# Performance work log

Hardware: AMD Instinct MI355X
Metric: run time of the kernel (lower is better)

## Reference

```python
import jax, jax.numpy as jnp
import numpy as np

TEMPERATURE = 1.0
D_THRESH = 0.1
EPS = 1e-10
NORM_EPS = 1e-12  # F.normalize clamp


def _l2_normalize(x):
    n = jnp.sqrt(jnp.sum(x * x, axis=1, keepdims=True))
    return x / jnp.maximum(n, NORM_EPS)


def setup_inputs() -> dict:
    key = jax.random.key(0)
    k1, k2, k3 = jax.random.split(key, 3)
    N, D = 8192, 128
    f1 = jax.random.normal(k1, (N, D), dtype=jnp.float32)
    f2 = jax.random.normal(k2, (N, D), dtype=jnp.float32)
    # continuous targets in [-1, 1) so both the distance mask (|ti-tj|>0.1)
    # and the polarity mask (sign mismatch) are exercised
    targets = jax.random.uniform(k3, (N,), dtype=jnp.float32, minval=-1.0, maxval=1.0)
    return {"f1": f1, "f2": f2, "targets": targets}


def reference(f1, f2, targets):
    f1 = _l2_normalize(f1)
    f2 = _l2_normalize(f2)

    # self_mask: 1 where pair is a negative (far target or opposite polarity)
    dist_t = jnp.abs(targets[:, None] - targets[None, :])  # [N,N]
    mask_distance = dist_t > D_THRESH
    polarity = targets > 0
    mask_polarity = polarity[:, None] != polarity[None, :]
    self_mask = (mask_distance | mask_polarity).astype(f1.dtype)  # [N,N]

    # ||f1_i - f2_j||^2 via the cdist/matmul trick (avoids [N,N,D] tensor)
    sq1 = jnp.sum(f1 * f1, axis=1)  # [N]
    sq2 = jnp.sum(f2 * f2, axis=1)  # [N]
    dist = sq1[:, None] - 2.0 * (f1 @ f2.T) + sq2[None, :]  # [N,N]
    cos = 1.0 - 0.5 * dist

    p = jax.nn.softmax(cos / TEMPERATURE, axis=1)  # [N,N]
    pos_w = 1.0 - self_mask
    log_pos = -jnp.log(p + EPS) * pos_w
    log_neg = -jnp.log(1.0 - p + EPS) * self_mask
    per_row = (jnp.sum(log_pos, axis=1) / jnp.sum(pos_w, axis=1)
               + jnp.sum(log_neg, axis=1) / jnp.sum(self_mask, axis=1))
    return jnp.mean(per_row)
```

## Files before the change

### kernel.cpp

```cpp
#include <hip/hip_runtime.h>
#include <hip/hip_bf16.h>
#include <math.h>

#define NROWS 8192
#define DDIM  128
#define JCHUNKS 16
#define JPER  (NROWS / JCHUNKS)
#define STAGE_COLS 64
#define NSTAGES (JPER / STAGE_COLS)
#define ROWS_PER_BLOCK 128
#define GRIDX (NROWS / ROWS_PER_BLOCK)
#define LOG2E 1.44269504088896f

#define AS1 __attribute__((address_space(1)))
#define AS3 __attribute__((address_space(3)))

typedef __attribute__((ext_vector_type(8))) short bf16x8;
typedef __attribute__((ext_vector_type(4))) float f32x4;

__global__ __launch_bounds__(256) void norm_kernel(
    const float* __restrict__ f1, const float* __restrict__ f2,
    __hip_bfloat16* __restrict__ f1b, __hip_bfloat16* __restrict__ f2b,
    float* __restrict__ out) {
  if (blockIdx.x == 0 && threadIdx.x == 0) out[0] = 0.0f;
  int t = threadIdx.x;
  int rloc = t >> 5;
  int l = t & 31;
  int b = blockIdx.x;
  int half = (b >= NROWS / 8) ? 1 : 0;
  int row = (b - half * (NROWS / 8)) * 8 + rloc;
  const float* src = half ? f2 : f1;
  __hip_bfloat16* dst = half ? f2b : f1b;

  float4 v = ((const float4*)src)[row * (DDIM / 4) + l];
  float s = v.x * v.x + v.y * v.y + v.z * v.z + v.w * v.w;
  #pragma unroll
  for (int off = 1; off < 32; off <<= 1) s += __shfl_xor(s, off, 64);
  float inv = 1.0f / fmaxf(sqrtf(s), 1e-12f);
  __hip_bfloat16 hv[4];
  hv[0] = __float2bfloat16(v.x * inv);
  hv[1] = __float2bfloat16(v.y * inv);
  hv[2] = __float2bfloat16(v.z * inv);
  hv[3] = __float2bfloat16(v.w * inv);
  *(ushort4*)&dst[(size_t)row * DDIM + l * 4] = *(ushort4*)hv;
}

__global__ __launch_bounds__(128, 2) void stats_kernel(
    const __hip_bfloat16* __restrict__ f1b,
    const __hip_bfloat16* __restrict__ f2b,
    const float* __restrict__ targets,
    float* __restrict__ partials) {
  __shared__ __align__(16) char lds0[STAGE_COLS * 256];
  __shared__ __align__(16) char lds1[STAGE_COLS * 256];
  __shared__ __align__(16) float tsh[JPER];

  const int chunk = blockIdx.y;
  const int i0 = blockIdx.x * ROWS_PER_BLOCK;
  const int w    = threadIdx.x >> 6;
  const int lane = threadIdx.x & 63;
  const int p15  = lane & 15;
  const int rl4  = lane >> 4;
  const int rbase = i0 + w * 64;

  bf16x8 afrag[4][4];
  #pragma unroll
  for (int rs = 0; rs < 4; ++rs) {
    const __hip_bfloat16* arow =
        &f1b[(size_t)(rbase + rs * 16 + p15) * DDIM + rl4 * 8];
    #pragma unroll
    for (int ks = 0; ks < 4; ++ks)
      afrag[rs][ks] = *(const bf16x8*)(arow + ks * 32);
  }

  f32x4 ki[4];
  #pragma unroll
  for (int rs = 0; rs < 4; ++rs)
    #pragma unroll
    for (int rr = 0; rr < 4; ++rr)
      ki[rs][rr] = targets[rbase + rs * 16 + rl4 * 4 + rr];

  f32x4 Z[4], Zp[4], Cp[4], Np[4];
  #pragma unroll
  for (int rs = 0; rs < 4; ++rs) {
    Z[rs] = (f32x4){0.f, 0.f, 0.f, 0.f};
    Zp[rs] = (f32x4){0.f, 0.f, 0.f, 0.f};
    Cp[rs] = (f32x4){0.f, 0.f, 0.f, 0.f};
    Np[rs] = (f32x4){0.f, 0.f, 0.f, 0.f};
  }

  const int jb0 = chunk * JPER;

  int srcoff[8];
  #pragma unroll
  for (int q = 0; q < 8; ++q) {
    int rloc = w * 32 + q * 4 + rl4;
    int c    = p15 ^ ((q * 4 + rl4) & 15);
    srcoff[q] = rloc * DDIM + c * 8;
  }

  {
    #pragma unroll
    for (int rnd = 0; rnd < 4; ++rnd)
      __builtin_amdgcn_global_load_lds(
          (const AS1 void*)(targets + jb0 + rnd * 128 + threadIdx.x),
          (AS3 void*)(&tsh[rnd * 128 + w * 64]), 4, 0, 0);
    const __hip_bfloat16* gstage = f2b + (size_t)jb0 * DDIM;
    char* lbase = &lds0[w * 8192];
    #pragma unroll
    for (int q = 0; q < 8; ++q)
      __builtin_amdgcn_global_load_lds((const AS1 void*)(gstage + srcoff[q]),
                                       (AS3 void*)(lbase + q * 1024), 16, 0, 0);
  }

  for (int s = 0; s < NSTAGES; ++s) {
    __syncthreads();

    if (s + 1 < NSTAGES) {
      const __hip_bfloat16* gstage = f2b + (size_t)(jb0 + (s + 1) * STAGE_COLS) * DDIM;
      char* lbase = ((s + 1) & 1) ? &lds1[w * 8192] : &lds0[w * 8192];
      #pragma unroll
      for (int q = 0; q < 8; ++q)
        __builtin_amdgcn_global_load_lds((const AS1 void*)(gstage + srcoff[q]),
                                         (AS3 void*)(lbase + q * 1024), 16, 0, 0);
    }

    const char* lb = (s & 1) ? lds1 : lds0;
    #pragma unroll
    for (int ct = 0; ct < 4; ++ct) {
      const int rloc = ct * 16 + p15;
      bf16x8 bfrag[4];
      #pragma unroll
      for (int ks = 0; ks < 4; ++ks)
        bfrag[ks] = *(const bf16x8*)(lb + rloc * 256 + (((rl4 + ks * 4) ^ p15) << 4));

      float tj = tsh[s * STAGE_COLS + ct * 16 + p15];
      const bool pj = tj > 0.0f;
      const f32x4 tj4 = {tj, tj, tj, tj};
      const f32x4 K4  = {LOG2E, LOG2E, LOG2E, LOG2E};

      #pragma unroll
      for (int rs = 0; rs < 4; ++rs) {
        f32x4 acc = {0.f, 0.f, 0.f, 0.f};
        #pragma unroll
        for (int ks = 0; ks < 4; ++ks)
          acc = __builtin_amdgcn_mfma_f32_16x16x32_bf16(afrag[rs][ks], bfrag[ks], acc, 0, 0, 0);

        f32x4 c4 = acc;
        f32x4 d4 = ki[rs] - tj4;
        f32x4 m4;
        #pragma unroll
        for (int rr = 0; rr < 4; ++rr) {
          bool q = (__builtin_fabsf(d4[rr]) <= 0.1f) & ((ki[rs][rr] > 0.0f) == pj);
          m4[rr] = q ? 1.0f : 0.0f;
        }
        f32x4 x4 = c4 * K4 - K4;
        f32x4 e4;
        #pragma unroll
        for (int rr = 0; rr < 4; ++rr) e4[rr] = __builtin_amdgcn_exp2f(x4[rr]);
        Z[rs]  += e4;
        Zp[rs] += m4 * e4;
        Cp[rs] += m4 * c4;
        Np[rs] += m4;
      }
    }
  }

  #pragma unroll
  for (int rs = 0; rs < 4; ++rs) {
    #pragma unroll
    for (int rr = 0; rr < 4; ++rr) {
      #pragma unroll
      for (int off = 1; off < 16; off <<= 1) {
        Z[rs][rr]  += __shfl_xor(Z[rs][rr],  off, 64);
        Zp[rs][rr] += __shfl_xor(Zp[rs][rr], off, 64);
        Cp[rs][rr] += __shfl_xor(Cp[rs][rr], off, 64);
        Np[rs][rr] += __shfl_xor(Np[rs][rr], off, 64);
      }
    }
  }
  if (p15 == 0) {
    #pragma unroll
    for (int rs = 0; rs < 4; ++rs)
      #pragma unroll
      for (int rr = 0; rr < 4; ++rr) {
        size_t row = rbase + rs * 16 + rl4 * 4 + rr;
        f32x4 st = {Z[rs][rr], Zp[rs][rr], Cp[rs][rr], Np[rs][rr]};
        *(f32x4*)&partials[((size_t)row * JCHUNKS + chunk) * 4] = st;
      }
  }
}

__global__ void finalize_rows(const float* __restrict__ partials,
                              float* __restrict__ out) {
  int r = blockIdx.x * 256 + threadIdx.x;
  float Z = 0, Zp = 0, Cp = 0, Np = 0;
  for (int ch = 0; ch < JCHUNKS; ++ch) {
    float4 p = *(const float4*)&partials[((size_t)r * JCHUNKS + ch) * 4];
    Z += p.x; Zp += p.y; Cp += p.z; Np += p.w;
  }
  float Zn = Z - Zp;
  float nn = (float)NROWS - Np;
  float spos = (1.0f + logf(Z)) - Cp / Np;
  float sneg = Zn / Z - nn * 1e-10f;
  float per_row = spos + sneg / nn;

  float v = per_row;
  for (int off = 32; off; off >>= 1) v += __shfl_xor(v, off, 64);
  __shared__ float wsum[4];
  int lane = threadIdx.x & 63, wid = threadIdx.x >> 6;
  if (lane == 0) wsum[wid] = v;
  __syncthreads();
  if (threadIdx.x == 0)
    atomicAdd(out, (wsum[0] + wsum[1] + wsum[2] + wsum[3]) * (1.0f / (float)NROWS));
}

extern "C" void kernel_launch(void* const* d_in, const int* in_sizes, int n_in,
                              void* d_out, int out_size, void* d_ws, size_t ws_size,
                              hipStream_t stream) {
  const float* f1  = (const float*)d_in[0];
  const float* f2  = (const float*)d_in[1];
  const float* tgt = (const float*)d_in[2];
  float* out = (float*)d_out;

  char* ws = (char*)d_ws;
  __hip_bfloat16* f1b = (__hip_bfloat16*)ws;
  __hip_bfloat16* f2b = (__hip_bfloat16*)(ws + (size_t)NROWS * DDIM * 2);
  float* partials = (float*)(ws + (size_t)NROWS * DDIM * 4);

  norm_kernel<<<2 * (NROWS / 8), 256, 0, stream>>>(f1, f2, f1b, f2b, out);
  dim3 g2(GRIDX, JCHUNKS);
  stats_kernel<<<g2, 128, 0, stream>>>(f1b, f2b, tgt, partials);
  finalize_rows<<<NROWS / 256, 256, 0, stream>>>(partials, out);
}
```

Before: 102.3 us.

## Load B fragments directly from global into registers, drop LDS staging

Removes the LDS double-buffered staging of f2 tiles and targets, along with the per-stage __syncthreads. Each wave now loads its B fragments and target values straight from global memory into registers, using a two-deep software-pipelined register double buffer. This cuts LDS traffic and block-wide barriers. In exchange, the two waves in a block each fetch the same B data from global/L2 separately, and latency hiding now depends on the register prefetch alone.

```diff
diff --git a/kernel.cpp b/kernel.cpp
--- a/kernel.cpp
+++ b/kernel.cpp
@@ -6,14 +6,10 @@
 #define DDIM  128
 #define JCHUNKS 16
 #define JPER  (NROWS / JCHUNKS)
-#define STAGE_COLS 64
-#define NSTAGES (JPER / STAGE_COLS)
+#define CT_TOTAL (JPER / 16)
 #define ROWS_PER_BLOCK 128
 #define GRIDX (NROWS / ROWS_PER_BLOCK)
 #define LOG2E 1.44269504088896f
-
-#define AS1 __attribute__((address_space(1)))
-#define AS3 __attribute__((address_space(3)))
 
 typedef __attribute__((ext_vector_type(8))) short bf16x8;
 typedef __attribute__((ext_vector_type(4))) float f32x4;
@@ -50,10 +46,6 @@
     const __hip_bfloat16* __restrict__ f2b,
     const float* __restrict__ targets,
     float* __restrict__ partials) {
-  __shared__ __align__(16) char lds0[STAGE_COLS * 256];
-  __shared__ __align__(16) char lds1[STAGE_COLS * 256];
-  __shared__ __align__(16) float tsh[JPER];
-
   const int chunk = blockIdx.y;
   const int i0 = blockIdx.x * ROWS_PER_BLOCK;
   const int w    = threadIdx.x >> 6;
@@ -89,81 +81,63 @@
   }
 
   const int jb0 = chunk * JPER;
-
-  int srcoff[8];
-  #pragma unroll
-  for (int q = 0; q < 8; ++q) {
-    int rloc = w * 32 + q * 4 + rl4;
-    int c    = p15 ^ ((q * 4 + rl4) & 15);
-    srcoff[q] = rloc * DDIM + c * 8;
-  }
-
-  {
-    #pragma unroll
-    for (int rnd = 0; rnd < 4; ++rnd)
-      __builtin_amdgcn_global_load_lds(
-          (const AS1 void*)(targets + jb0 + rnd * 128 + threadIdx.x),
-          (AS3 void*)(&tsh[rnd * 128 + w * 64]), 4, 0, 0);
-    const __hip_bfloat16* gstage = f2b + (size_t)jb0 * DDIM;
-    char* lbase = &lds0[w * 8192];
-    #pragma unroll
-    for (int q = 0; q < 8; ++q)
-      __builtin_amdgcn_global_load_lds((const AS1 void*)(gstage + srcoff[q]),
-                                       (AS3 void*)(lbase + q * 1024), 16, 0, 0);
-  }
-
-  for (int s = 0; s < NSTAGES; ++s) {
-    __syncthreads();
-
-    if (s + 1 < NSTAGES) {
-      const __hip_bfloat16* gstage = f2b + (size_t)(jb0 + (s + 1) * STAGE_COLS) * DDIM;
-      char* lbase = ((s + 1) & 1) ? &lds1[w * 8192] : &lds0[w * 8192];
-      #pragma unroll
-      for (int q = 0; q < 8; ++q)
-        __builtin_amdgcn_global_load_lds((const AS1 void*)(gstage + srcoff[q]),
-                                         (AS3 void*)(lbase + q * 1024), 16, 0, 0);
-    }
-
-    const char* lb = (s & 1) ? lds1 : lds0;
-    #pragma unroll
-    for (int ct = 0; ct < 4; ++ct) {
-      const int rloc = ct * 16 + p15;
-      bf16x8 bfrag[4];
-      #pragma unroll
-      for (int ks = 0; ks < 4; ++ks)
-        bfrag[ks] = *(const bf16x8*)(lb + rloc * 256 + (((rl4 + ks * 4) ^ p15) << 4));
-
-      float tj = tsh[s * STAGE_COLS + ct * 16 + p15];
-      const bool pj = tj > 0.0f;
-      const f32x4 tj4 = {tj, tj, tj, tj};
-      const f32x4 K4  = {LOG2E, LOG2E, LOG2E, LOG2E};
-
-      #pragma unroll
-      for (int rs = 0; rs < 4; ++rs) {
-        f32x4 acc = {0.f, 0.f, 0.f, 0.f};
-        #pragma unroll
-        for (int ks = 0; ks < 4; ++ks)
-          acc = __builtin_amdgcn_mfma_f32_16x16x32_bf16(afrag[rs][ks], bfrag[ks], acc, 0, 0, 0);
-
-        f32x4 c4 = acc;
-        f32x4 d4 = ki[rs] - tj4;
-        f32x4 m4;
-        #pragma unroll
-        for (int rr = 0; rr < 4; ++rr) {
-          bool q = (__builtin_fabsf(d4[rr]) <= 0.1f) & ((ki[rs][rr] > 0.0f) == pj);
-          m4[rr] = q ? 1.0f : 0.0f;
-        }
-        f32x4 x4 = c4 * K4 - K4;
-        f32x4 e4;
-        #pragma unroll
-        for (int rr = 0; rr < 4; ++rr) e4[rr] = __builtin_amdgcn_exp2f(x4[rr]);
-        Z[rs]  += e4;
-        Zp[rs] += m4 * e4;
-        Cp[rs] += m4 * c4;
-        Np[rs] += m4;
-      }
-    }
-  }
+  const __hip_bfloat16* bptr = f2b + (size_t)(jb0 + p15) * DDIM + rl4 * 8;
+  const float* tptr = targets + jb0 + p15;
+
+  #define LOADB(BF, TJ, CT)                                                 \
+    do {                                                                    \
+      const __hip_bfloat16* _p = bptr + (size_t)(CT) * 16 * DDIM;           \
+      _Pragma("unroll")                                                     \
+      for (int _ks = 0; _ks < 4; ++_ks)                                     \
+        (BF)[_ks] = *(const bf16x8*)(_p + _ks * 32);                        \
+      (TJ) = tptr[(CT) * 16];                                               \
+    } while (0)
+
+  #define COMPUTE(BF, TJ)                                                   \
+    do {                                                                    \
+      const float _tj = (TJ);                                               \
+      const bool _pj = _tj > 0.0f;                                          \
+      const f32x4 _tj4 = {_tj, _tj, _tj, _tj};                              \
+      const f32x4 _K4  = {LOG2E, LOG2E, LOG2E, LOG2E};                      \
+      _Pragma("unroll")                                                     \
+      for (int _rs = 0; _rs < 4; ++_rs) {                                   \
+        f32x4 _acc = {0.f, 0.f, 0.f, 0.f};                                  \
+        _Pragma("unroll")                                                   \
+        for (int _ks = 0; _ks < 4; ++_ks)                                   \
+          _acc = __builtin_amdgcn_mfma_f32_16x16x32_bf16(                   \
+              afrag[_rs][_ks], (BF)[_ks], _acc, 0, 0, 0);                   \
+        f32x4 _c4 = _acc;                                                   \
+        f32x4 _d4 = ki[_rs] - _tj4;                                         \
+        f32x4 _m4;                                                          \
+        _Pragma("unroll")                                                   \
+        for (int _rr = 0; _rr < 4; ++_rr) {                                 \
+          bool _q = (__builtin_fabsf(_d4[_rr]) <= 0.1f) &                   \
+                    ((ki[_rs][_rr] > 0.0f) == _pj);                         \
+          _m4[_rr] = _q ? 1.0f : 0.0f;                                      \
+        }                                                                   \
+        f32x4 _x4 = _c4 * _K4 - _K4;                                        \
+        f32x4 _e4;                                                          \
+        _Pragma("unroll")                                                   \
+        for (int _rr = 0; _rr < 4; ++_rr)                                   \
+          _e4[_rr] = __builtin_amdgcn_exp2f(_x4[_rr]);                      \
+        Z[_rs]  += _e4;                                                     \
+        Zp[_rs] += _m4 * _e4;                                               \
+        Cp[_rs] += _m4 * _c4;                                               \
+        Np[_rs] += _m4;                                                     \
+      }                                                                     \
+    } while (0)
+
+  bf16x8 bA[4], bB[4];
+  float tjA, tjB;
+  LOADB(bA, tjA, 0);
+  for (int ct = 0; ct < CT_TOTAL; ct += 2) {
+    LOADB(bB, tjB, ct + 1);
+    COMPUTE(bA, tjA);
+    if (ct + 2 < CT_TOTAL) LOADB(bA, tjA, ct + 2);
+    COMPUTE(bB, tjB);
+  }
+  #undef LOADB
+  #undef COMPUTE
 
   #pragma unroll
   for (int rs = 0; rs < 4; ++rs) {
```

Result: slower. 106.9 us (+4.5%).
